# Performance work log

Hardware: AMD Instinct MI355X
Metric: run time of the kernel (lower is better)

The kernel has to match this reference:

```python
import jax, jax.numpy as jnp
import numpy as np

EPS = 1e-5  # torch GroupNorm default


def group_norm(x, num_groups):
    # x: [B, C]; normalize within each group of C // num_groups channels (biased var)
    B, C = x.shape
    xg = x.reshape(B, num_groups, C // num_groups)
    mean = jnp.mean(xg, axis=-1, keepdims=True)
    var = jnp.var(xg, axis=-1, keepdims=True)
    return ((xg - mean) * jax.lax.rsqrt(var + EPS)).reshape(B, C)


def setup_inputs() -> dict:
    key = jax.random.key(0)
    ks = jax.random.split(key, 8)
    B, D_IN, H = 16384, 512, 512
    x = jax.random.normal(ks[0], (B, D_IN), dtype=jnp.float32)
    h = jax.random.normal(ks[1], (B, H), dtype=jnp.float32)
    c = jax.random.normal(ks[2], (B, H), dtype=jnp.float32)
    u = jax.random.normal(ks[3], (B, 8 * H), dtype=jnp.float32)
    # Linear(input_dim + hidden_dim -> 4 * hidden_dim), PyTorch default init scale
    fan_in = D_IN + H
    bound = 1.0 / np.sqrt(fan_in)
    W = jax.random.uniform(ks[4], (fan_in, 4 * H), jnp.float32, -bound, bound)
    b_lin = jax.random.uniform(ks[5], (4 * H,), jnp.float32, -bound, bound)
    # output_norm affine params (GroupNorm init: weight=1, bias=0)
    gamma = jnp.ones((H,), dtype=jnp.float32)
    beta = jnp.zeros((H,), dtype=jnp.float32)
    return {"x": x, "h": h, "c": c, "u": u, "W": W, "b_lin": b_lin,
            "gamma": gamma, "beta": beta}


def reference(x, h, c, u, W, b_lin, gamma, beta):
    # z = GroupNorm_4(Linear(cat(x, h)))  -> [B, 4H]
    z = jnp.concatenate((x, h), axis=1) @ W + b_lin
    z = group_norm(z, num_groups=4)
    # FiLM conditioning
    a, b = jnp.split(u, 2, axis=1)  # each [B, 4H]
    z = z * (1.0 + a) + b
    # LSTM gates
    i, f, o, g = jnp.split(z, 4, axis=1)  # each [B, H]
    c_new = jax.nn.sigmoid(f) * c + jax.nn.sigmoid(i) * jnp.tanh(g)
    # output_norm: GroupNorm(num_groups=1) with affine over H channels
    cn = group_norm(c_new, num_groups=1) * gamma + beta
    h_new = jax.nn.sigmoid(o) * jnp.tanh(cn)
    return h_new, c_new
```

## Files before the change

### kernel.cpp

```cpp
#include <hip/hip_runtime.h>
#include <hip/hip_bf16.h>
#include <math.h>


typedef __attribute__((ext_vector_type(8))) short bf16x8;
typedef __attribute__((ext_vector_type(4))) float f32x4;

static constexpr int Bn = 16384;
static constexpr int K  = 1024;
static constexpr int N  = 2048;
static constexpr int H  = 512;

__device__ __forceinline__ unsigned short f2bf(float f) {
  unsigned int u = __builtin_bit_cast(unsigned int, f);
  u += 0x7FFFu + ((u >> 16) & 1u);
  return (unsigned short)(u >> 16);
}
__device__ __forceinline__ float bf2f(unsigned short s) {
  unsigned int u = ((unsigned int)s) << 16;
  return __builtin_bit_cast(float, u);
}

__global__ void prep_a(const float* __restrict__ x, const float* __restrict__ h,
                       unsigned short* __restrict__ A) {
  const int total = Bn * (K / 4);
  for (int idx = blockIdx.x * blockDim.x + threadIdx.x; idx < total;
       idx += gridDim.x * blockDim.x) {
    int row = idx >> 8;
    int k = (idx & 255) * 4;
    const float* src = (k < 512) ? (x + (size_t)row * 512 + k)
                                 : (h + (size_t)row * 512 + (k - 512));
    float4 v = *reinterpret_cast<const float4*>(src);
    ushort4 o;
    o.x = f2bf(v.x); o.y = f2bf(v.y); o.z = f2bf(v.z); o.w = f2bf(v.w);
    *reinterpret_cast<ushort4*>(A + (size_t)row * K + k) = o;
  }
}

__global__ void prep_bt(const float* __restrict__ W, unsigned short* __restrict__ Bt) {
  __shared__ unsigned short tile[32][33];
  const int n0 = blockIdx.x * 32;
  const int k0 = blockIdx.y * 32;
  const int tx = threadIdx.x;
  const int ty = threadIdx.y;
#pragma unroll
  for (int i = 0; i < 4; i++) {
    int k = k0 + ty + i * 8;
    tile[ty + i * 8][tx] = f2bf(W[(size_t)k * N + n0 + tx]);
  }
  __syncthreads();
#pragma unroll
  for (int i = 0; i < 4; i++) {
    int n = n0 + ty + i * 8;
    Bt[(size_t)n * K + k0 + tx] = tile[tx][ty + i * 8];
  }
}

__global__ __launch_bounds__(256, 2) void gemm_bt(
    const unsigned short* __restrict__ A,
    const unsigned short* __restrict__ Bt,
    const float* __restrict__ blin,
    unsigned short* __restrict__ Z) {
  __shared__ unsigned short As[128 * 32];
  __shared__ unsigned short Bs[128 * 32];
  const int tid = threadIdx.x;
  const int lane = tid & 63;
  const int wid = tid >> 6;
  const int wr = wid >> 1, wc = wid & 1;
  const int m0 = blockIdx.y * 128;
  const int n0 = blockIdx.x * 128;
  const int l15 = lane & 15;
  const int lk = (lane >> 4) * 8;

  f32x4 acc[4][4] = {};

  for (int k0 = 0; k0 < K; k0 += 32) {
    __syncthreads();
#pragma unroll
    for (int j = 0; j < 2; j++) {
      int t = j * 256 + tid;
      int row = t >> 2;
      int col = (t & 3) * 8;
      *reinterpret_cast<int4*>(&As[row * 32 + col]) =
          *reinterpret_cast<const int4*>(&A[(size_t)(m0 + row) * K + k0 + col]);
      *reinterpret_cast<int4*>(&Bs[row * 32 + col]) =
          *reinterpret_cast<const int4*>(&Bt[(size_t)(n0 + row) * K + k0 + col]);
    }
    __syncthreads();
    bf16x8 a[4], b[4];
#pragma unroll
    for (int fm = 0; fm < 4; fm++)
      a[fm] = *reinterpret_cast<const bf16x8*>(&As[(wr * 64 + fm * 16 + l15) * 32 + lk]);
#pragma unroll
    for (int fn = 0; fn < 4; fn++)
      b[fn] = *reinterpret_cast<const bf16x8*>(&Bs[(wc * 64 + fn * 16 + l15) * 32 + lk]);
#pragma unroll
    for (int fm = 0; fm < 4; fm++)
#pragma unroll
      for (int fn = 0; fn < 4; fn++)
        acc[fm][fn] = __builtin_amdgcn_mfma_f32_16x16x32_bf16(a[fm], b[fn], acc[fm][fn], 0, 0, 0);
  }

  const int orow = (lane >> 4) * 4;
#pragma unroll
  for (int fm = 0; fm < 4; fm++) {
#pragma unroll
    for (int fn = 0; fn < 4; fn++) {
      int col = n0 + wc * 64 + fn * 16 + l15;
      float bl = blin[col];
#pragma unroll
      for (int j = 0; j < 4; j++) {
        int row = m0 + wr * 64 + fm * 16 + orow + j;
        Z[(size_t)row * N + col] = f2bf(acc[fm][fn][j] + bl);
      }
    }
  }
}

__global__ __launch_bounds__(512) void fused_tail(
    const unsigned short* __restrict__ Z,
    const float* __restrict__ u,
    const float* __restrict__ c,
    const float* __restrict__ gamma, const float* __restrict__ beta,
    float* __restrict__ out) {
  const int m = blockIdx.x;
  const int j = threadIdx.x;
  const int lane = j & 63;
  const int wid = j >> 6;
  __shared__ float s_sum[4][8], s_sq[4][8];
  __shared__ float s2_sum[8], s2_sq[8];

  float zf[4];
#pragma unroll
  for (int g = 0; g < 4; g++)
    zf[g] = bf2f(Z[(size_t)m * N + g * H + j]);

#pragma unroll
  for (int g = 0; g < 4; g++) {
    float s = zf[g], q = zf[g] * zf[g];
#pragma unroll
    for (int off = 32; off >= 1; off >>= 1) {
      s += __shfl_xor(s, off, 64);
      q += __shfl_xor(q, off, 64);
    }
    if (lane == 0) { s_sum[g][wid] = s; s_sq[g][wid] = q; }
  }
  __syncthreads();
  float zfilm[4];
#pragma unroll
  for (int g = 0; g < 4; g++) {
    float s = 0.f, q = 0.f;
#pragma unroll
    for (int w = 0; w < 8; w++) { s += s_sum[g][w]; q += s_sq[g][w]; }
    float mu = s * (1.0f / 512.0f);
    float var = q * (1.0f / 512.0f) - mu * mu;
    float rs = rsqrtf(var + 1e-5f);
    float a = u[(size_t)m * 4096 + g * H + j];
    float b = u[(size_t)m * 4096 + 2048 + g * H + j];
    zfilm[g] = (zf[g] - mu) * rs * (1.0f + a) + b;
  }
  const float ig = 1.f / (1.f + expf(-zfilm[0]));
  const float fg = 1.f / (1.f + expf(-zfilm[1]));
  const float og = 1.f / (1.f + expf(-zfilm[2]));
  const float gg = tanhf(zfilm[3]);
  const float cnew = fg * c[(size_t)m * H + j] + ig * gg;

  {
    float s = cnew, q = cnew * cnew;
#pragma unroll
    for (int off = 32; off >= 1; off >>= 1) {
      s += __shfl_xor(s, off, 64);
      q += __shfl_xor(q, off, 64);
    }
    if (lane == 0) { s2_sum[wid] = s; s2_sq[wid] = q; }
  }
  __syncthreads();
  float s = 0.f, q = 0.f;
#pragma unroll
  for (int w = 0; w < 8; w++) { s += s2_sum[w]; q += s2_sq[w]; }
  float mu = s * (1.0f / 512.0f);
  float var = q * (1.0f / 512.0f) - mu * mu;
  float cnorm = (cnew - mu) * rsqrtf(var + 1e-5f) * gamma[j] + beta[j];
  float hn = og * tanhf(cnorm);

  out[(size_t)m * H + j] = hn;
  out[(size_t)Bn * H + (size_t)m * H + j] = cnew;
}

extern "C" void kernel_launch(void* const* d_in, const int* in_sizes, int n_in,
                              void* d_out, int out_size, void* d_ws, size_t ws_size,
                              hipStream_t stream) {
  const float* x     = (const float*)d_in[0];
  const float* h     = (const float*)d_in[1];
  const float* c     = (const float*)d_in[2];
  const float* u     = (const float*)d_in[3];
  const float* W     = (const float*)d_in[4];
  const float* blin  = (const float*)d_in[5];
  const float* gamma = (const float*)d_in[6];
  const float* beta  = (const float*)d_in[7];
  float* out = (float*)d_out;

  unsigned short* A  = (unsigned short*)d_ws;
  unsigned short* Bt = A + (size_t)Bn * K;
  unsigned short* Z  = Bt + (size_t)N * K;

  prep_a<<<2048, 256, 0, stream>>>(x, h, A);
  prep_bt<<<dim3(N / 32, K / 32), dim3(32, 8), 0, stream>>>(W, Bt);
  gemm_bt<<<dim3(N / 128, Bn / 128), 256, 0, stream>>>(A, Bt, blin, Z);
  fused_tail<<<Bn, 512, 0, stream>>>(Z, u, c, gamma, beta, out);
}
```

Measured before the change: 571.6 us.

## Use direct global-to-LDS loads, LDS-staged GEMM epilogue, wave-per-row tail

The GEMM now loads A and B tiles with global_load_lds, which writes straight into LDS and skips the trip through registers. Its epilogue writes results to an LDS buffer first, then stores them to Z in coalesced 16-byte rows. The tail kernel is rewritten so one wavefront handles a whole row with 8 elements per lane, which removes block-level syncs. It also uses vector float4 loads and fast __expf-based sigmoid and tanh. The fast math can lose accuracy, and the larger LDS allocation may reduce GEMM occupancy.

Result: faster. 533.9 us (-6.6%).

```diff
diff --git a/kernel.cpp b/kernel.cpp
--- a/kernel.cpp
+++ b/kernel.cpp
@@ -19,6 +19,12 @@
 __device__ __forceinline__ float bf2f(unsigned short s) {
   unsigned int u = ((unsigned int)s) << 16;
   return __builtin_bit_cast(float, u);
+}
+__device__ __forceinline__ float fsig(float x) {
+  return 1.0f / (1.0f + __expf(-x));
+}
+__device__ __forceinline__ float ftanh(float x) {
+  return 1.0f - 2.0f / (1.0f + __expf(2.0f * x));
 }
 
 __global__ void prep_a(const float* __restrict__ x, const float* __restrict__ h,
@@ -61,8 +67,9 @@
     const unsigned short* __restrict__ Bt,
     const float* __restrict__ blin,
     unsigned short* __restrict__ Z) {
-  __shared__ unsigned short As[128 * 32];
-  __shared__ unsigned short Bs[128 * 32];
+  __shared__ unsigned short smem[128 * 136];
+  unsigned short* As = smem;
+  unsigned short* Bs = smem + 128 * 32;
   const int tid = threadIdx.x;
   const int lane = tid & 63;
   const int wid = tid >> 6;
@@ -78,13 +85,15 @@
     __syncthreads();
 #pragma unroll
     for (int j = 0; j < 2; j++) {
-      int t = j * 256 + tid;
-      int row = t >> 2;
-      int col = (t & 3) * 8;
-      *reinterpret_cast<int4*>(&As[row * 32 + col]) =
-          *reinterpret_cast<const int4*>(&A[(size_t)(m0 + row) * K + k0 + col]);
-      *reinterpret_cast<int4*>(&Bs[row * 32 + col]) =
-          *reinterpret_cast<const int4*>(&Bt[(size_t)(n0 + row) * K + k0 + col]);
+      int item = j * 256 + tid;
+      int row = item >> 2;
+      int kb = (item & 3) * 8;
+      __builtin_amdgcn_global_load_lds(
+          (const __attribute__((address_space(1))) void*)&A[(size_t)(m0 + row) * K + k0 + kb],
+          (__attribute__((address_space(3))) void*)&As[item * 8], 16, 0, 0);
+      __builtin_amdgcn_global_load_lds(
+          (const __attribute__((address_space(1))) void*)&Bt[(size_t)(n0 + row) * K + k0 + kb],
+          (__attribute__((address_space(3))) void*)&Bs[item * 8], 16, 0, 0);
     }
     __syncthreads();
     bf16x8 a[4], b[4];
@@ -101,90 +110,112 @@
         acc[fm][fn] = __builtin_amdgcn_mfma_f32_16x16x32_bf16(a[fm], b[fn], acc[fm][fn], 0, 0, 0);
   }
 
+  __syncthreads();
   const int orow = (lane >> 4) * 4;
 #pragma unroll
-  for (int fm = 0; fm < 4; fm++) {
-#pragma unroll
-    for (int fn = 0; fn < 4; fn++) {
-      int col = n0 + wc * 64 + fn * 16 + l15;
-      float bl = blin[col];
+  for (int fn = 0; fn < 4; fn++) {
+    float bl = blin[n0 + wc * 64 + fn * 16 + l15];
+#pragma unroll
+    for (int fm = 0; fm < 4; fm++) {
 #pragma unroll
       for (int j = 0; j < 4; j++) {
-        int row = m0 + wr * 64 + fm * 16 + orow + j;
-        Z[(size_t)row * N + col] = f2bf(acc[fm][fn][j] + bl);
+        smem[(wr * 64 + fm * 16 + orow + j) * 136 + wc * 64 + fn * 16 + l15] =
+            f2bf(acc[fm][fn][j] + bl);
       }
     }
   }
-}
-
-__global__ __launch_bounds__(512) void fused_tail(
+  __syncthreads();
+#pragma unroll
+  for (int it = 0; it < 8; it++) {
+    int item = it * 256 + tid;
+    int row = item >> 4;
+    int cb = (item & 15) * 8;
+    int4 v = *reinterpret_cast<const int4*>(&smem[row * 136 + cb]);
+    *reinterpret_cast<int4*>(&Z[(size_t)(m0 + row) * N + n0 + cb]) = v;
+  }
+}
+
+__global__ __launch_bounds__(256) void fused_tail(
     const unsigned short* __restrict__ Z,
     const float* __restrict__ u,
     const float* __restrict__ c,
     const float* __restrict__ gamma, const float* __restrict__ beta,
     float* __restrict__ out) {
-  const int m = blockIdx.x;
-  const int j = threadIdx.x;
-  const int lane = j & 63;
-  const int wid = j >> 6;
-  __shared__ float s_sum[4][8], s_sq[4][8];
-  __shared__ float s2_sum[8], s2_sq[8];
-
-  float zf[4];
-#pragma unroll
-  for (int g = 0; g < 4; g++)
-    zf[g] = bf2f(Z[(size_t)m * N + g * H + j]);
-
+  const int lane = threadIdx.x & 63;
+  const int m = blockIdx.x * 4 + (threadIdx.x >> 6);
+  const int j0 = lane * 8;
+
+  float zfilm[4][8];
 #pragma unroll
   for (int g = 0; g < 4; g++) {
-    float s = zf[g], q = zf[g] * zf[g];
+    bf16x8 v = *reinterpret_cast<const bf16x8*>(&Z[(size_t)m * N + g * H + j0]);
+    float zf[8];
+    float s = 0.f, q = 0.f;
+#pragma unroll
+    for (int r = 0; r < 8; r++) {
+      zf[r] = bf2f((unsigned short)v[r]);
+      s += zf[r]; q += zf[r] * zf[r];
+    }
 #pragma unroll
     for (int off = 32; off >= 1; off >>= 1) {
       s += __shfl_xor(s, off, 64);
       q += __shfl_xor(q, off, 64);
     }
-    if (lane == 0) { s_sum[g][wid] = s; s_sq[g][wid] = q; }
-  }
-  __syncthreads();
-  float zfilm[4];
-#pragma unroll
-  for (int g = 0; g < 4; g++) {
-    float s = 0.f, q = 0.f;
-#pragma unroll
-    for (int w = 0; w < 8; w++) { s += s_sum[g][w]; q += s_sq[g][w]; }
     float mu = s * (1.0f / 512.0f);
-    float var = q * (1.0f / 512.0f) - mu * mu;
-    float rs = rsqrtf(var + 1e-5f);
-    float a = u[(size_t)m * 4096 + g * H + j];
-    float b = u[(size_t)m * 4096 + 2048 + g * H + j];
-    zfilm[g] = (zf[g] - mu) * rs * (1.0f + a) + b;
-  }
-  const float ig = 1.f / (1.f + expf(-zfilm[0]));
-  const float fg = 1.f / (1.f + expf(-zfilm[1]));
-  const float og = 1.f / (1.f + expf(-zfilm[2]));
-  const float gg = tanhf(zfilm[3]);
-  const float cnew = fg * c[(size_t)m * H + j] + ig * gg;
-
-  {
-    float s = cnew, q = cnew * cnew;
-#pragma unroll
-    for (int off = 32; off >= 1; off >>= 1) {
-      s += __shfl_xor(s, off, 64);
-      q += __shfl_xor(q, off, 64);
-    }
-    if (lane == 0) { s2_sum[wid] = s; s2_sq[wid] = q; }
-  }
-  __syncthreads();
+    float rs = rsqrtf(q * (1.0f / 512.0f) - mu * mu + 1e-5f);
+    float4 a0 = *reinterpret_cast<const float4*>(&u[(size_t)m * 4096 + g * H + j0]);
+    float4 a1 = *reinterpret_cast<const float4*>(&u[(size_t)m * 4096 + g * H + j0 + 4]);
+    float4 b0 = *reinterpret_cast<const float4*>(&u[(size_t)m * 4096 + 2048 + g * H + j0]);
+    float4 b1 = *reinterpret_cast<const float4*>(&u[(size_t)m * 4096 + 2048 + g * H + j0 + 4]);
+    float af[8] = {a0.x, a0.y, a0.z, a0.w, a1.x, a1.y, a1.z, a1.w};
+    float bf[8] = {b0.x, b0.y, b0.z, b0.w, b1.x, b1.y, b1.z, b1.w};
+#pragma unroll
+    for (int r = 0; r < 8; r++)
+      zfilm[g][r] = (zf[r] - mu) * rs * (1.0f + af[r]) + bf[r];
+  }
+
+  float4 c0 = *reinterpret_cast<const float4*>(&c[(size_t)m * H + j0]);
+  float4 c1 = *reinterpret_cast<const float4*>(&c[(size_t)m * H + j0 + 4]);
+  float cold[8] = {c0.x, c0.y, c0.z, c0.w, c1.x, c1.y, c1.z, c1.w};
+  float cnew[8], og[8];
   float s = 0.f, q = 0.f;
 #pragma unroll
-  for (int w = 0; w < 8; w++) { s += s2_sum[w]; q += s2_sq[w]; }
+  for (int r = 0; r < 8; r++) {
+    float ig = fsig(zfilm[0][r]);
+    float fg = fsig(zfilm[1][r]);
+    og[r] = fsig(zfilm[2][r]);
+    float gg = ftanh(zfilm[3][r]);
+    cnew[r] = fg * cold[r] + ig * gg;
+    s += cnew[r]; q += cnew[r] * cnew[r];
+  }
+#pragma unroll
+  for (int off = 32; off >= 1; off >>= 1) {
+    s += __shfl_xor(s, off, 64);
+    q += __shfl_xor(q, off, 64);
+  }
   float mu = s * (1.0f / 512.0f);
-  float var = q * (1.0f / 512.0f) - mu * mu;
-  float cnorm = (cnew - mu) * rsqrtf(var + 1e-5f) * gamma[j] + beta[j];
-  float hn = og * tanhf(cnorm);
-
-  out[(size_t)m * H + j] = hn;
-  out[(size_t)Bn * H + (size_t)m * H + j] = cnew;
+  float rs = rsqrtf(q * (1.0f / 512.0f) - mu * mu + 1e-5f);
+
+  float4 g0 = *reinterpret_cast<const float4*>(&gamma[j0]);
+  float4 g1 = *reinterpret_cast<const float4*>(&gamma[j0 + 4]);
+  float4 e0 = *reinterpret_cast<const float4*>(&beta[j0]);
+  float4 e1 = *reinterpret_cast<const float4*>(&beta[j0 + 4]);
+  float gam[8] = {g0.x, g0.y, g0.z, g0.w, g1.x, g1.y, g1.z, g1.w};
+  float bet[8] = {e0.x, e0.y, e0.z, e0.w, e1.x, e1.y, e1.z, e1.w};
+  float hn[8];
+#pragma unroll
+  for (int r = 0; r < 8; r++) {
+    float cn = (cnew[r] - mu) * rs * gam[r] + bet[r];
+    hn[r] = og[r] * ftanh(cn);
+  }
+  float4 h0 = {hn[0], hn[1], hn[2], hn[3]};
+  float4 h1 = {hn[4], hn[5], hn[6], hn[7]};
+  float4 cn0 = {cnew[0], cnew[1], cnew[2], cnew[3]};
+  float4 cn1 = {cnew[4], cnew[5], cnew[6], cnew[7]};
+  *reinterpret_cast<float4*>(&out[(size_t)m * H + j0]) = h0;
+  *reinterpret_cast<float4*>(&out[(size_t)m * H + j0 + 4]) = h1;
+  *reinterpret_cast<float4*>(&out[(size_t)Bn * H + (size_t)m * H + j0]) = cn0;
+  *reinterpret_cast<float4*>(&out[(size_t)Bn * H + (size_t)m * H + j0 + 4]) = cn1;
 }
 
 extern "C" void kernel_launch(void* const* d_in, const int* in_sizes, int n_in,
@@ -207,5 +238,5 @@
   prep_a<<<2048, 256, 0, stream>>>(x, h, A);
   prep_bt<<<dim3(N / 32, K / 32), dim3(32, 8), 0, stream>>>(W, Bt);
   gemm_bt<<<dim3(N / 128, Bn / 128), 256, 0, stream>>>(A, Bt, blin, Z);
-  fused_tail<<<Bn, 512, 0, stream>>>(Z, u, c, gamma, beta, out);
-}
+  fused_tail<<<Bn / 4, 256, 0, stream>>>(Z, u, c, gamma, beta, out);
+}
```
